# Optimization experiments

Hardware: AMD Instinct MI355X
Metric: run time of the kernel (lower is better)

The kernel has to match this reference:

```python
import jax, jax.numpy as jnp
import numpy as np


def setup_inputs() -> dict:
    key = jax.random.key(0)
    k1, k2, k3, k4 = jax.random.split(key, 4)
    T, IN, OUT = 4096, 4096, 4096  # tokens, in_features, out_features
    x = jax.random.normal(k1, (T, IN), dtype=jnp.float32)
    # simulated FP8 weight values (already quantized integers-ish codes stored as float)
    weight = jax.random.normal(k2, (OUT, IN), dtype=jnp.float32)
    # per-output-channel dequant scale
    weight_scale = jax.random.uniform(k3, (OUT,), dtype=jnp.float32, minval=0.01, maxval=0.1)
    bias = jax.random.normal(k4, (OUT,), dtype=jnp.float32)
    return {"x": x, "weight": weight, "weight_scale": weight_scale, "bias": bias}


def reference(x, weight, weight_scale, bias) -> jnp.ndarray:
    # FP8 quantized linear: dequantize weight with per-channel scale, then GEMM + bias.
    # weight: [out, in], weight_scale: [out], x: [tokens, in] -> out: [tokens, out]
    w_deq = weight * weight_scale[:, None]
    return jnp.einsum("ti,oi->to", x, w_deq) + bias
```

## Files before the change

kernel.cpp:

```cpp
#include <hip/hip_runtime.h>
#include <hip/hip_bf16.h>
#include <stdint.h>

typedef __bf16 bf16_t;
typedef bf16_t bf16x8 __attribute__((ext_vector_type(8)));
typedef float f32x4 __attribute__((ext_vector_type(4)));

#define BM 256
#define BN 256
#define BK 64

__device__ __forceinline__ void gload_lds16(const void* g, void* l) {
  __builtin_amdgcn_global_load_lds(
      (const __attribute__((address_space(1))) uint32_t*)g,
      (__attribute__((address_space(3))) uint32_t*)l, 16, 0, 0);
}

__global__ __launch_bounds__(256) void cvt_kernel(
    const float* __restrict__ x, bf16_t* __restrict__ xo, int n8x,
    const float* __restrict__ w, const float* __restrict__ scale,
    bf16_t* __restrict__ wo, int k8, int n8w, int gx) {
  if ((int)blockIdx.x < gx) {
    int stride = gx * blockDim.x;
    for (int i = blockIdx.x * blockDim.x + threadIdx.x; i < n8x; i += stride) {
      const f32x4* p = (const f32x4*)x + 2 * (size_t)i;
      f32x4 a = p[0], b = p[1];
      bf16x8 o;
#pragma unroll
      for (int r = 0; r < 4; ++r) { o[r] = (bf16_t)a[r]; o[r + 4] = (bf16_t)b[r]; }
      *((bf16x8*)xo + i) = o;
    }
  } else {
    int stride = (gridDim.x - gx) * blockDim.x;
    for (int i = (blockIdx.x - gx) * blockDim.x + threadIdx.x; i < n8w;
         i += stride) {
      int row = i / k8;
      float s = scale[row];
      const f32x4* p = (const f32x4*)w + 2 * (size_t)i;
      f32x4 a = p[0], b = p[1];
      bf16x8 o;
#pragma unroll
      for (int r = 0; r < 4; ++r) {
        o[r] = (bf16_t)(a[r] * s);
        o[r + 4] = (bf16_t)(b[r] * s);
      }
      *((bf16x8*)wo + i) = o;
    }
  }
}

__global__ __launch_bounds__(512, 2) void gemm256(
    const bf16_t* __restrict__ A, const bf16_t* __restrict__ B,
    const float* __restrict__ bias, float* __restrict__ C,
    int M, int N, int K) {
  __shared__ __attribute__((aligned(16))) char lds[131072];

  const int tid = threadIdx.x;
  const int lane = tid & 63;
  const int wave = tid >> 6;
  const int wm = wave >> 2;
  const int wn = wave & 3;

  int nwg = gridDim.x;
  int wg = blockIdx.x;
  if ((nwg & 7) == 0) { int cpx = nwg >> 3; wg = (wg & 7) * cpx + (wg >> 3); }
  const int ntn = N / BN;
  const int tm = wg / ntn;
  const int tn = wg % ntn;

  const size_t Kb = (size_t)K * 2;
  const char* gApan = (const char*)A + (size_t)tm * BM * Kb;
  const char* gBpan = (const char*)B + (size_t)tn * BN * Kb;

  const int xc = (((lane >> 4) ^ ((lane >> 1) & 3)) << 4);
  const int aBase = (wm * 128 + (lane & 15)) * 64 + xc;
  const int bBase = (wn * 64 + (lane & 15)) * 64 + xc;

  size_t srcoff[2];
  int ldst[2];
#pragma unroll
  for (int s = 0; s < 2; ++s) {
    int r = (wave * 2 + s) * 16 + (lane >> 2);
    int c = (lane & 3) ^ ((lane >> 3) & 3);
    srcoff[s] = (size_t)r * Kb + (size_t)(c << 4);
    ldst[s] = (wave * 2 + s) * 1024;
  }

#define STAGE_U(dstbase, pan, kbyte)                                          \
  {                                                                           \
    gload_lds16((pan) + srcoff[0] + (size_t)(kbyte), lds + (dstbase) + ldst[0]); \
    gload_lds16((pan) + srcoff[1] + (size_t)(kbyte), lds + (dstbase) + ldst[1]); \
  }
#define RD_A(dst, unitbase, ch)                                               \
  _Pragma("unroll") for (int i_ = 0; i_ < 4; ++i_)                            \
      dst[i_] = *(const bf16x8*)(lds + (unitbase) + aBase + (ch) * 4096 +     \
                                 i_ * 1024);
#define RD_B(dst, unitbase)                                                   \
  _Pragma("unroll") for (int j_ = 0; j_ < 4; ++j_)                            \
      dst[j_] = *(const bf16x8*)(lds + (unitbase) + bBase + j_ * 1024);
#define MFMA16(ab, bb_, accbase)                                              \
  __builtin_amdgcn_s_setprio(1);                                              \
  _Pragma("unroll") for (int i_ = 0; i_ < 4; ++i_)                            \
      _Pragma("unroll") for (int j_ = 0; j_ < 4; ++j_)                        \
          acc[(accbase) + i_][j_] = __builtin_amdgcn_mfma_f32_16x16x32_bf16(  \
              ab[i_], bb_[j_], acc[(accbase) + i_][j_], 0, 0, 0);             \
  __builtin_amdgcn_s_setprio(0);
#define WAIT_LGKM0() asm volatile("s_waitcnt lgkmcnt(0)" ::: "memory")
#define WAIT_VM(n)   asm volatile("s_waitcnt vmcnt(" #n ")" ::: "memory")
#define BAR()        __builtin_amdgcn_s_barrier()

  f32x4 acc[8][4];
#pragma unroll
  for (int a = 0; a < 8; ++a)
#pragma unroll
    for (int j = 0; j < 4; ++j) acc[a][j] = (f32x4)0.0f;

  const int NT = K / BK;

  STAGE_U(0,             gApan, 0);
  STAGE_U(32768,         gBpan, 0);
  STAGE_U(16384,         gApan, 64);
  STAGE_U(49152,         gBpan, 64);
  if (NT > 1) {
    STAGE_U(65536,         gApan, 128);
    STAGE_U(65536 + 32768, gBpan, 128);
    WAIT_VM(4);
  } else {
    WAIT_VM(0);
  }
  BAR();

  bf16x8 af[4], bf[4];

  for (int t = 0; t < NT; ++t) {
    const int bb = (t & 1) << 16;
    const int nb = bb ^ 65536;
    const size_t kb1 = (size_t)(t + 1) * 128;
    const size_t kb2 = (size_t)(t + 2) * 128;
    const bool st1 = (t + 1) < NT;
    const bool st2 = (t + 2) < NT;

    RD_A(af, bb, 0);
    RD_B(bf, bb + 32768);
    if (st1) STAGE_U(nb + 16384, gApan, kb1 + 64);
    BAR();
    WAIT_LGKM0();
    MFMA16(af, bf, 0);
    BAR();

    RD_A(af, bb, 1);
    if (st1) STAGE_U(nb + 49152, gBpan, kb1 + 64);
    BAR();
    WAIT_LGKM0();
    MFMA16(af, bf, 4);
    BAR();

    RD_A(af, bb + 16384, 0);
    RD_B(bf, bb + 49152);
    if (st2) STAGE_U(bb, gApan, kb2);
    BAR();
    WAIT_LGKM0();
    MFMA16(af, bf, 0);
    BAR();

    RD_A(af, bb + 16384, 1);
    if (st2) STAGE_U(bb + 32768, gBpan, kb2);
    BAR();
    WAIT_LGKM0();
    MFMA16(af, bf, 4);
    if (st2) { WAIT_VM(4); } else { WAIT_VM(0); }
    BAR();
  }
#undef STAGE_U
#undef RD_A
#undef RD_B
#undef MFMA16
#undef WAIT_LGKM0
#undef WAIT_VM
#undef BAR

  const int row0 = tm * BM + wm * 128;
  const int col0 = tn * BN + wn * 64;
#pragma unroll
  for (int j = 0; j < 4; ++j) {
    int c = col0 + j * 16 + (lane & 15);
    float bv = bias[c];
#pragma unroll
    for (int a = 0; a < 8; ++a) {
      int ch = a >> 2, i = a & 3;
      int rbase = row0 + ch * 64 + i * 16 + ((lane >> 4) << 2);
#pragma unroll
      for (int r = 0; r < 4; ++r)
        C[(size_t)(rbase + r) * N + c] = acc[a][j][r] + bv;
    }
  }
}

__global__ void fallback_gemm(const float* __restrict__ x,
                              const float* __restrict__ w,
                              const float* __restrict__ s,
                              const float* __restrict__ b,
                              float* __restrict__ out, int M, int N, int K) {
  int o = blockIdx.x * blockDim.x + threadIdx.x;
  if (o >= M * N) return;
  int m = o / N, n = o % N;
  const float* xr = x + (size_t)m * K;
  const float* wr = w + (size_t)n * K;
  float acc = 0.f;
  for (int k = 0; k < K; ++k) acc += xr[k] * wr[k];
  out[o] = acc * s[n] + b[n];
}

extern "C" void kernel_launch(void* const* d_in, const int* in_sizes, int n_in,
                              void* d_out, int out_size, void* d_ws,
                              size_t ws_size, hipStream_t stream) {
  const float* x = (const float*)d_in[0];
  const float* w = (const float*)d_in[1];
  const float* sc = (const float*)d_in[2];
  const float* bias = (const float*)d_in[3];
  float* out = (float*)d_out;

  const int N = in_sizes[2];
  const int K = in_sizes[1] / N;
  const int M = in_sizes[0] / K;

  const size_t need = ((size_t)M * K + (size_t)N * K) * sizeof(bf16_t);
  const bool fast = (ws_size >= need) && (M % BM == 0) && (N % BN == 0) &&
                    (K % BK == 0) && (K / BK >= 1);

  if (fast) {
    bf16_t* xb = (bf16_t*)d_ws;
    bf16_t* wb = xb + (size_t)M * K;

    int n8x = (M * K) / 8;
    int n8w = (N * K) / 8;
    const int gx = 2048;
    cvt_kernel<<<gx + 2048, 256, 0, stream>>>(x, xb, n8x, w, sc, wb, K / 8,
                                              n8w, gx);

    dim3 grid((M / BM) * (N / BN));
    gemm256<<<grid, 512, 0, stream>>>(xb, wb, bias, out, M, N, K);
  } else {
    int total = M * N;
    fallback_gemm<<<(total + 255) / 256, 256, 0, stream>>>(x, w, sc, bias, out,
                                                           M, N, K);
  }
}
```

Before: 158.9 us.

## Switch GEMM to 32x32x16 MFMA with double-buffered A fragments and fewer barriers

Replaces the 16x16x32 bf16 MFMA tiling with 32x32x16 instructions, which makes each wave issue fewer, larger MFMAs and read fewer LDS fragments per FLOP. The main loop is restructured from four barrier-separated phases into two. A-fragment register double buffering (aX/aY) prefetches the next k-slice's A operand while the current MFMAs run. Partial lgkmcnt waits and sched_barriers are used to keep LDS reads in flight. This adds register pressure from the extra A buffers and depends on the new swizzled LDS addressing being correct.

```diff
diff --git a/kernel.cpp b/kernel.cpp
--- a/kernel.cpp
+++ b/kernel.cpp
@@ -5,6 +5,7 @@
 typedef __bf16 bf16_t;
 typedef bf16_t bf16x8 __attribute__((ext_vector_type(8)));
 typedef float f32x4 __attribute__((ext_vector_type(4)));
+typedef float f32x16 __attribute__((ext_vector_type(16)));
 
 #define BM 256
 #define BN 256
@@ -72,9 +73,12 @@
   const char* gApan = (const char*)A + (size_t)tm * BM * Kb;
   const char* gBpan = (const char*)B + (size_t)tn * BN * Kb;
 
-  const int xc = (((lane >> 4) ^ ((lane >> 1) & 3)) << 4);
-  const int aBase = (wm * 128 + (lane & 15)) * 64 + xc;
-  const int bBase = (wn * 64 + (lane & 15)) * 64 + xc;
+  const int xs = (lane >> 1) & 3;
+  const int hi = lane >> 5;
+  const int cs0 = ((hi ^ xs) << 4);
+  const int cs1 = (((hi + 2) ^ xs) << 4);
+  const int aAddr = wm * 8192 + (lane & 31) * 64;
+  const int bAddr = wn * 4096 + (lane & 31) * 64;
 
   size_t srcoff[2];
   int ldst[2];
@@ -91,107 +95,111 @@
     gload_lds16((pan) + srcoff[0] + (size_t)(kbyte), lds + (dstbase) + ldst[0]); \
     gload_lds16((pan) + srcoff[1] + (size_t)(kbyte), lds + (dstbase) + ldst[1]); \
   }
-#define RD_A(dst, unitbase, ch)                                               \
-  _Pragma("unroll") for (int i_ = 0; i_ < 4; ++i_)                            \
-      dst[i_] = *(const bf16x8*)(lds + (unitbase) + aBase + (ch) * 4096 +     \
-                                 i_ * 1024);
-#define RD_B(dst, unitbase)                                                   \
-  _Pragma("unroll") for (int j_ = 0; j_ < 4; ++j_)                            \
-      dst[j_] = *(const bf16x8*)(lds + (unitbase) + bBase + j_ * 1024);
-#define MFMA16(ab, bb_, accbase)                                              \
+#define STAGE_K0(buf, tt)                                                     \
+  { STAGE_U((buf) + 0,     gApan, (size_t)(tt)*128);                          \
+    STAGE_U((buf) + 32768, gBpan, (size_t)(tt)*128); }
+#define STAGE_K1(buf, tt)                                                     \
+  { STAGE_U((buf) + 16384, gApan, (size_t)(tt)*128 + 64);                     \
+    STAGE_U((buf) + 49152, gBpan, (size_t)(tt)*128 + 64); }
+#define RD_B4(ub)                                                             \
+  _Pragma("unroll") for (int fc_ = 0; fc_ < 2; ++fc_) {                       \
+    bfr[fc_][0] = *(const bf16x8*)(lds + (ub) + bAddr + fc_ * 2048 + cs0);    \
+    bfr[fc_][1] = *(const bf16x8*)(lds + (ub) + bAddr + fc_ * 2048 + cs1);    \
+  }
+#define RD_A8(dst, ub)                                                        \
+  _Pragma("unroll") for (int fr_ = 0; fr_ < 4; ++fr_) {                       \
+    dst[fr_][0] = *(const bf16x8*)(lds + (ub) + aAddr + fr_ * 2048 + cs0);    \
+    dst[fr_][1] = *(const bf16x8*)(lds + (ub) + aAddr + fr_ * 2048 + cs1);    \
+  }
+#define MFMA16(aU)                                                            \
   __builtin_amdgcn_s_setprio(1);                                              \
-  _Pragma("unroll") for (int i_ = 0; i_ < 4; ++i_)                            \
-      _Pragma("unroll") for (int j_ = 0; j_ < 4; ++j_)                        \
-          acc[(accbase) + i_][j_] = __builtin_amdgcn_mfma_f32_16x16x32_bf16(  \
-              ab[i_], bb_[j_], acc[(accbase) + i_][j_], 0, 0, 0);             \
+  _Pragma("unroll") for (int fr_ = 0; fr_ < 4; ++fr_)                         \
+      _Pragma("unroll") for (int fc_ = 0; fc_ < 2; ++fc_) {                   \
+        acc[fr_][fc_] = __builtin_amdgcn_mfma_f32_32x32x16_bf16(              \
+            aU[fr_][0], bfr[fc_][0], acc[fr_][fc_], 0, 0, 0);                 \
+        acc[fr_][fc_] = __builtin_amdgcn_mfma_f32_32x32x16_bf16(              \
+            aU[fr_][1], bfr[fc_][1], acc[fr_][fc_], 0, 0, 0);                 \
+      }                                                                       \
   __builtin_amdgcn_s_setprio(0);
-#define WAIT_LGKM0() asm volatile("s_waitcnt lgkmcnt(0)" ::: "memory")
+#define WAIT_LGKM(n) asm volatile("s_waitcnt lgkmcnt(" #n ")" ::: "memory")
 #define WAIT_VM(n)   asm volatile("s_waitcnt vmcnt(" #n ")" ::: "memory")
+#define SCHED0()     __builtin_amdgcn_sched_barrier(0)
 #define BAR()        __builtin_amdgcn_s_barrier()
 
-  f32x4 acc[8][4];
-#pragma unroll
-  for (int a = 0; a < 8; ++a)
-#pragma unroll
-    for (int j = 0; j < 4; ++j) acc[a][j] = (f32x4)0.0f;
+  f32x16 acc[4][2];
+#pragma unroll
+  for (int fr = 0; fr < 4; ++fr)
+#pragma unroll
+    for (int fc = 0; fc < 2; ++fc) acc[fr][fc] = (f32x16)0.0f;
 
   const int NT = K / BK;
 
-  STAGE_U(0,             gApan, 0);
-  STAGE_U(32768,         gBpan, 0);
-  STAGE_U(16384,         gApan, 64);
-  STAGE_U(49152,         gBpan, 64);
+  STAGE_K0(0, 0);
+  STAGE_K1(0, 0);
   if (NT > 1) {
-    STAGE_U(65536,         gApan, 128);
-    STAGE_U(65536 + 32768, gBpan, 128);
+    STAGE_K0(65536, 1);
     WAIT_VM(4);
   } else {
     WAIT_VM(0);
   }
+  SCHED0();
   BAR();
 
-  bf16x8 af[4], bf[4];
+  bf16x8 aX[4][2], aY[4][2], bfr[2][2];
+  RD_A8(aX, 0);
 
   for (int t = 0; t < NT; ++t) {
     const int bb = (t & 1) << 16;
     const int nb = bb ^ 65536;
-    const size_t kb1 = (size_t)(t + 1) * 128;
-    const size_t kb2 = (size_t)(t + 2) * 128;
     const bool st1 = (t + 1) < NT;
     const bool st2 = (t + 2) < NT;
 
-    RD_A(af, bb, 0);
-    RD_B(bf, bb + 32768);
-    if (st1) STAGE_U(nb + 16384, gApan, kb1 + 64);
+    RD_B4(bb + 32768);
+    RD_A8(aY, bb + 16384);
+    if (st1) STAGE_K1(nb, t + 1);
+    WAIT_LGKM(8);
+    SCHED0();
+    MFMA16(aX);
+    if (st1) { WAIT_VM(4); } else { WAIT_VM(0); }
+    SCHED0();
     BAR();
-    WAIT_LGKM0();
-    MFMA16(af, bf, 0);
+
+    RD_B4(bb + 49152);
+    if (st1) RD_A8(aX, nb);
+    if (st2) STAGE_K0(bb, t + 2);
+    if (st1) { WAIT_LGKM(8); } else { WAIT_LGKM(0); }
+    SCHED0();
+    MFMA16(aY);
+    if (st2) { WAIT_VM(4); } else { WAIT_VM(0); }
+    SCHED0();
     BAR();
-
-    RD_A(af, bb, 1);
-    if (st1) STAGE_U(nb + 49152, gBpan, kb1 + 64);
-    BAR();
-    WAIT_LGKM0();
-    MFMA16(af, bf, 4);
-    BAR();
-
-    RD_A(af, bb + 16384, 0);
-    RD_B(bf, bb + 49152);
-    if (st2) STAGE_U(bb, gApan, kb2);
-    BAR();
-    WAIT_LGKM0();
-    MFMA16(af, bf, 0);
-    BAR();
-
-    RD_A(af, bb + 16384, 1);
-    if (st2) STAGE_U(bb + 32768, gBpan, kb2);
-    BAR();
-    WAIT_LGKM0();
-    MFMA16(af, bf, 4);
-    if (st2) { WAIT_VM(4); } else { WAIT_VM(0); }
-    BAR();
   }
 #undef STAGE_U
-#undef RD_A
-#undef RD_B
+#undef STAGE_K0
+#undef STAGE_K1
+#undef RD_B4
+#undef RD_A8
 #undef MFMA16
-#undef WAIT_LGKM0
+#undef WAIT_LGKM
 #undef WAIT_VM
+#undef SCHED0
 #undef BAR
 
   const int row0 = tm * BM + wm * 128;
   const int col0 = tn * BN + wn * 64;
-#pragma unroll
-  for (int j = 0; j < 4; ++j) {
-    int c = col0 + j * 16 + (lane & 15);
+  const int lrow = (lane >> 5) << 2;
+  const int lcol = lane & 31;
+#pragma unroll
+  for (int fc = 0; fc < 2; ++fc) {
+    int c = col0 + fc * 32 + lcol;
     float bv = bias[c];
 #pragma unroll
-    for (int a = 0; a < 8; ++a) {
-      int ch = a >> 2, i = a & 3;
-      int rbase = row0 + ch * 64 + i * 16 + ((lane >> 4) << 2);
-#pragma unroll
-      for (int r = 0; r < 4; ++r)
-        C[(size_t)(rbase + r) * N + c] = acc[a][j][r] + bv;
+    for (int fr = 0; fr < 4; ++fr) {
+#pragma unroll
+      for (int reg = 0; reg < 16; ++reg) {
+        int r = row0 + fr * 32 + (reg & 3) + ((reg >> 2) << 3) + lrow;
+        C[(size_t)r * N + c] = acc[fr][fc][reg] + bv;
+      }
     }
   }
 }
```

After: 172.6 us. 1.09x slower.

## Double-buffer LDS fragment registers to overlap reads with MFMA in GEMM loop

Applied to the files above, without the earlier changes.

Restructures the GEMM main loop to use two sets of A/B register fragments, so the LDS reads for the next MFMA block are issued before the current MFMA block runs. Full lgkmcnt(0) waits and one barrier per phase are replaced by partial waits and a single barrier. The loop is unrolled by two with precomputed LDS base pointers for each buffer, which requires an even tile count. The goal is to hide LDS read latency behind matrix math and cut synchronisation, at the cost of more registers and tighter ordering constraints.

```diff
diff --git a/kernel.cpp b/kernel.cpp
--- a/kernel.cpp
+++ b/kernel.cpp
@@ -75,6 +75,10 @@
   const int xc = (((lane >> 4) ^ ((lane >> 1) & 3)) << 4);
   const int aBase = (wm * 128 + (lane & 15)) * 64 + xc;
   const int bBase = (wn * 64 + (lane & 15)) * 64 + xc;
+  const char* pA0 = lds + aBase;
+  const char* pA1 = lds + 65536 + aBase;
+  const char* pB0 = lds + bBase;
+  const char* pB1 = lds + 65536 + bBase;
 
   size_t srcoff[2];
   int ldst[2];
@@ -86,18 +90,17 @@
     ldst[s] = (wave * 2 + s) * 1024;
   }
 
-#define STAGE_U(dstbase, pan, kbyte)                                          \
+#define STAGE_U(dstc, pan, kbyte)                                             \
   {                                                                           \
-    gload_lds16((pan) + srcoff[0] + (size_t)(kbyte), lds + (dstbase) + ldst[0]); \
-    gload_lds16((pan) + srcoff[1] + (size_t)(kbyte), lds + (dstbase) + ldst[1]); \
-  }
-#define RD_A(dst, unitbase, ch)                                               \
+    gload_lds16((pan) + srcoff[0] + (size_t)(kbyte), lds + (dstc) + ldst[0]); \
+    gload_lds16((pan) + srcoff[1] + (size_t)(kbyte), lds + (dstc) + ldst[1]); \
+  }
+#define RD_A(dst, P, u, ch)                                                   \
   _Pragma("unroll") for (int i_ = 0; i_ < 4; ++i_)                            \
-      dst[i_] = *(const bf16x8*)(lds + (unitbase) + aBase + (ch) * 4096 +     \
-                                 i_ * 1024);
-#define RD_B(dst, unitbase)                                                   \
+      dst[i_] = *(const bf16x8*)((P) + (u) + (ch) * 4096 + i_ * 1024);
+#define RD_B(dst, P, u)                                                       \
   _Pragma("unroll") for (int j_ = 0; j_ < 4; ++j_)                            \
-      dst[j_] = *(const bf16x8*)(lds + (unitbase) + bBase + j_ * 1024);
+      dst[j_] = *(const bf16x8*)((P) + (u) + j_ * 1024);
 #define MFMA16(ab, bb_, accbase)                                              \
   __builtin_amdgcn_s_setprio(1);                                              \
   _Pragma("unroll") for (int i_ = 0; i_ < 4; ++i_)                            \
@@ -105,9 +108,44 @@
           acc[(accbase) + i_][j_] = __builtin_amdgcn_mfma_f32_16x16x32_bf16(  \
               ab[i_], bb_[j_], acc[(accbase) + i_][j_], 0, 0, 0);             \
   __builtin_amdgcn_s_setprio(0);
-#define WAIT_LGKM0() asm volatile("s_waitcnt lgkmcnt(0)" ::: "memory")
+#define WAIT_LGKM(n) asm volatile("s_waitcnt lgkmcnt(" #n ")" ::: "memory")
 #define WAIT_VM(n)   asm volatile("s_waitcnt vmcnt(" #n ")" ::: "memory")
 #define BAR()        __builtin_amdgcn_s_barrier()
+
+#define TILE(t_, aBB, bBB, aNB, bNB, BBc, NBc)                                \
+  {                                                                           \
+    const bool st1 = (t_) + 1 < NT;                                           \
+    const bool st2 = (t_) + 2 < NT;                                           \
+    const size_t kb1 = (size_t)((t_) + 1) * 128;                              \
+    const size_t kb2 = (size_t)((t_) + 2) * 128;                              \
+                               \
+    if (st1) STAGE_U((NBc) + 16384, gApan, kb1 + 64);                         \
+    RD_A(aY, aBB, 0, 1);                                                      \
+    WAIT_LGKM(4);                                                             \
+    MFMA16(aX, b0, 0);                                                        \
+    BAR();                                                                    \
+                    \
+    if (st1) STAGE_U((NBc) + 49152, gBpan, kb1 + 64);                         \
+    RD_A(aX, aBB, 16384, 0);                                                  \
+    RD_B(b1, bBB, 49152);                                                     \
+    WAIT_LGKM(8);                                                             \
+    MFMA16(aY, b0, 4);                                                        \
+    BAR();                                                                    \
+                               \
+    if (st2) STAGE_U((BBc), gApan, kb2);                                      \
+    RD_A(aY, aBB, 16384, 1);                                                  \
+    WAIT_LGKM(4);                                                             \
+    MFMA16(aX, b1, 0);                                                        \
+    if (st2) { WAIT_VM(6); } else if (st1) { WAIT_VM(4); } else { WAIT_VM(0); } \
+    BAR();                                                                    \
+                           \
+    if (st2) STAGE_U((BBc) + 32768, gBpan, kb2);                              \
+    if (st1) { RD_A(aX, aNB, 0, 0); RD_B(b0, bNB, 32768); }                   \
+    if (st1) { WAIT_LGKM(8); } else { WAIT_LGKM(0); }                         \
+    MFMA16(aY, b1, 4);                                                        \
+    if (st2) { WAIT_VM(4); } else { WAIT_VM(0); }                             \
+    BAR();                                                                    \
+  }
 
   f32x4 acc[8][4];
 #pragma unroll
@@ -130,54 +168,22 @@
   }
   BAR();
 
-  bf16x8 af[4], bf[4];
-
-  for (int t = 0; t < NT; ++t) {
-    const int bb = (t & 1) << 16;
-    const int nb = bb ^ 65536;
-    const size_t kb1 = (size_t)(t + 1) * 128;
-    const size_t kb2 = (size_t)(t + 2) * 128;
-    const bool st1 = (t + 1) < NT;
-    const bool st2 = (t + 2) < NT;
-
-    RD_A(af, bb, 0);
-    RD_B(bf, bb + 32768);
-    if (st1) STAGE_U(nb + 16384, gApan, kb1 + 64);
-    BAR();
-    WAIT_LGKM0();
-    MFMA16(af, bf, 0);
-    BAR();
-
-    RD_A(af, bb, 1);
-    if (st1) STAGE_U(nb + 49152, gBpan, kb1 + 64);
-    BAR();
-    WAIT_LGKM0();
-    MFMA16(af, bf, 4);
-    BAR();
-
-    RD_A(af, bb + 16384, 0);
-    RD_B(bf, bb + 49152);
-    if (st2) STAGE_U(bb, gApan, kb2);
-    BAR();
-    WAIT_LGKM0();
-    MFMA16(af, bf, 0);
-    BAR();
-
-    RD_A(af, bb + 16384, 1);
-    if (st2) STAGE_U(bb + 32768, gBpan, kb2);
-    BAR();
-    WAIT_LGKM0();
-    MFMA16(af, bf, 4);
-    if (st2) { WAIT_VM(4); } else { WAIT_VM(0); }
-    BAR();
+  bf16x8 aX[4], aY[4], b0[4], b1[4];
+  RD_A(aX, pA0, 0, 0);
+  RD_B(b0, pB0, 32768);
+
+  for (int t = 0; t < NT; t += 2) {
+    TILE(t,     pA0, pB0, pA1, pB1, 0,     65536);
+    TILE(t + 1, pA1, pB1, pA0, pB0, 65536, 0);
   }
 #undef STAGE_U
 #undef RD_A
 #undef RD_B
 #undef MFMA16
-#undef WAIT_LGKM0
+#undef WAIT_LGKM
 #undef WAIT_VM
 #undef BAR
+#undef TILE
 
   const int row0 = tm * BM + wm * 128;
   const int col0 = tn * BN + wn * 64;
@@ -225,8 +231,9 @@
   const int M = in_sizes[0] / K;
 
   const size_t need = ((size_t)M * K + (size_t)N * K) * sizeof(bf16_t);
+  const int NT = K / BK;
   const bool fast = (ws_size >= need) && (M % BM == 0) && (N % BN == 0) &&
-                    (K % BK == 0) && (K / BK >= 1);
+                    (K % BK == 0) && (NT >= 2) && (NT % 2 == 0);
 
   if (fast) {
     bf16_t* xb = (bf16_t*)d_ws;
```

Measured after the change: 225.1 us. 41.7% more time.

## Restructure GEMM LDS layout to 128-byte rows and reorder quadrant MFMA schedule

Applied to the files above, without the earlier changes.

Changes the LDS tile layout from 64-byte K-half units to full 128-byte rows covering BK=64, split by row halves, with an 8-way XOR swizzle. Each fragment read now loads both K halves, and the main loop computes in four quadrants that reuse A and B fragments, so the final quadrant runs without a preceding LDS read and overlaps the next-stage prefetch. The goal is fewer LDS reads and barriers per iteration and better overlap of global-to-LDS loads. The cost is more live fragment registers, and the changed staging order could introduce hazards.

```diff
diff --git a/kernel.cpp b/kernel.cpp
--- a/kernel.cpp
+++ b/kernel.cpp
@@ -71,41 +71,61 @@
   const size_t Kb = (size_t)K * 2;
   const char* gApan = (const char*)A + (size_t)tm * BM * Kb;
   const char* gBpan = (const char*)B + (size_t)tn * BN * Kb;
-
-  const int xc = (((lane >> 4) ^ ((lane >> 1) & 3)) << 4);
-  const int aBase = (wm * 128 + (lane & 15)) * 64 + xc;
-  const int bBase = (wn * 64 + (lane & 15)) * 64 + xc;
+  const size_t rowHi = (size_t)128 * Kb;
+
+  const int l7 = lane & 7;
+  const int hi = lane >> 4;
+  const int c0b = ((hi ^ l7) << 4);
+  const int c1b = (((hi + 4) ^ l7) << 4);
+  const int aB0 = wm * 16384 + (lane & 15) * 128 + c0b;
+  const int aB1 = wm * 16384 + (lane & 15) * 128 + c1b;
+  const int bB0 = 32768 + (wn >> 1) * 16384 + (wn & 1) * 8192 +
+                  (lane & 15) * 128 + c0b;
+  const int bB1 = 32768 + (wn >> 1) * 16384 + (wn & 1) * 8192 +
+                  (lane & 15) * 128 + c1b;
 
   size_t srcoff[2];
   int ldst[2];
 #pragma unroll
   for (int s = 0; s < 2; ++s) {
-    int r = (wave * 2 + s) * 16 + (lane >> 2);
-    int c = (lane & 3) ^ ((lane >> 3) & 3);
-    srcoff[s] = (size_t)r * Kb + (size_t)(c << 4);
+    int row_l = (wave * 2 + s) * 8 + (lane >> 3);
+    int csrc = (lane & 7) ^ ((lane >> 3) & 7);
+    srcoff[s] = (size_t)row_l * Kb + (size_t)(csrc << 4);
     ldst[s] = (wave * 2 + s) * 1024;
   }
 
-#define STAGE_U(dstbase, pan, kbyte)                                          \
+#define STAGE_U(dstc, pan, rowoff, kbyte)                                     \
   {                                                                           \
-    gload_lds16((pan) + srcoff[0] + (size_t)(kbyte), lds + (dstbase) + ldst[0]); \
-    gload_lds16((pan) + srcoff[1] + (size_t)(kbyte), lds + (dstbase) + ldst[1]); \
-  }
-#define RD_A(dst, unitbase, ch)                                               \
-  _Pragma("unroll") for (int i_ = 0; i_ < 4; ++i_)                            \
-      dst[i_] = *(const bf16x8*)(lds + (unitbase) + aBase + (ch) * 4096 +     \
-                                 i_ * 1024);
-#define RD_B(dst, unitbase)                                                   \
-  _Pragma("unroll") for (int j_ = 0; j_ < 4; ++j_)                            \
-      dst[j_] = *(const bf16x8*)(lds + (unitbase) + bBase + j_ * 1024);
-#define MFMA16(ab, bb_, accbase)                                              \
+    gload_lds16((pan) + (rowoff) + srcoff[0] + (size_t)(kbyte),               \
+                lds + (dstc) + ldst[0]);                                      \
+    gload_lds16((pan) + (rowoff) + srcoff[1] + (size_t)(kbyte),               \
+                lds + (dstc) + ldst[1]);                                      \
+  }
+#define RD_A(r_)                                                              \
+  _Pragma("unroll") for (int i_ = 0; i_ < 4; ++i_) {                          \
+    af[i_][0] = *(const bf16x8*)(Lb + aB0 + (r_) * 8192 + i_ * 2048);         \
+    af[i_][1] = *(const bf16x8*)(Lb + aB1 + (r_) * 8192 + i_ * 2048);         \
+  }
+#define RD_BC(dst, c_)                                                        \
+  _Pragma("unroll") for (int j_ = 0; j_ < 2; ++j_) {                          \
+    dst[j_][0] = *(const bf16x8*)(Lb + bB0 + (c_) * 4096 + j_ * 2048);        \
+    dst[j_][1] = *(const bf16x8*)(Lb + bB1 + (c_) * 4096 + j_ * 2048);        \
+  }
+#define MFMAQ(r_, c_, bset)                                                   \
   __builtin_amdgcn_s_setprio(1);                                              \
   _Pragma("unroll") for (int i_ = 0; i_ < 4; ++i_)                            \
-      _Pragma("unroll") for (int j_ = 0; j_ < 4; ++j_)                        \
-          acc[(accbase) + i_][j_] = __builtin_amdgcn_mfma_f32_16x16x32_bf16(  \
-              ab[i_], bb_[j_], acc[(accbase) + i_][j_], 0, 0, 0);             \
+      _Pragma("unroll") for (int j_ = 0; j_ < 2; ++j_) {                      \
+        acc[(r_) * 4 + i_][(c_) * 2 + j_] =                                   \
+            __builtin_amdgcn_mfma_f32_16x16x32_bf16(                          \
+                af[i_][0], bset[j_][0], acc[(r_) * 4 + i_][(c_) * 2 + j_],    \
+                0, 0, 0);                                                     \
+        acc[(r_) * 4 + i_][(c_) * 2 + j_] =                                   \
+            __builtin_amdgcn_mfma_f32_16x16x32_bf16(                          \
+                af[i_][1], bset[j_][1], acc[(r_) * 4 + i_][(c_) * 2 + j_],    \
+                0, 0, 0);                                                     \
+      }                                                                       \
   __builtin_amdgcn_s_setprio(0);
-#define WAIT_LGKM0() asm volatile("s_waitcnt lgkmcnt(0)" ::: "memory")
+#define WAIT_LGKM(n) asm volatile("s_waitcnt lgkmcnt(" #n ")" ::: "memory")
 #define WAIT_VM(n)   asm volatile("s_waitcnt vmcnt(" #n ")" ::: "memory")
 #define BAR()        __builtin_amdgcn_s_barrier()
 
@@ -117,65 +137,65 @@
 
   const int NT = K / BK;
 
-  STAGE_U(0,             gApan, 0);
-  STAGE_U(32768,         gBpan, 0);
-  STAGE_U(16384,         gApan, 64);
-  STAGE_U(49152,         gBpan, 64);
+  STAGE_U(0,     gApan, 0,     0);
+  STAGE_U(16384, gApan, rowHi, 0);
+  STAGE_U(32768, gBpan, 0,     0);
+  STAGE_U(49152, gBpan, rowHi, 0);
   if (NT > 1) {
-    STAGE_U(65536,         gApan, 128);
-    STAGE_U(65536 + 32768, gBpan, 128);
+    STAGE_U(65536,         gApan, 0, 128);
+    STAGE_U(65536 + 32768, gBpan, 0, 128);
     WAIT_VM(4);
   } else {
     WAIT_VM(0);
   }
   BAR();
 
-  bf16x8 af[4], bf[4];
+  bf16x8 af[4][2], b0[2][2], b1[2][2];
 
   for (int t = 0; t < NT; ++t) {
     const int bb = (t & 1) << 16;
     const int nb = bb ^ 65536;
+    const char* Lb = lds + bb;
     const size_t kb1 = (size_t)(t + 1) * 128;
     const size_t kb2 = (size_t)(t + 2) * 128;
     const bool st1 = (t + 1) < NT;
     const bool st2 = (t + 2) < NT;
 
-    RD_A(af, bb, 0);
-    RD_B(bf, bb + 32768);
-    if (st1) STAGE_U(nb + 16384, gApan, kb1 + 64);
-    BAR();
-    WAIT_LGKM0();
-    MFMA16(af, bf, 0);
-    BAR();
-
-    RD_A(af, bb, 1);
-    if (st1) STAGE_U(nb + 49152, gBpan, kb1 + 64);
-    BAR();
-    WAIT_LGKM0();
-    MFMA16(af, bf, 4);
-    BAR();
-
-    RD_A(af, bb + 16384, 0);
-    RD_B(bf, bb + 49152);
-    if (st2) STAGE_U(bb, gApan, kb2);
-    BAR();
-    WAIT_LGKM0();
-    MFMA16(af, bf, 0);
-    BAR();
-
-    RD_A(af, bb + 16384, 1);
-    if (st2) STAGE_U(bb + 32768, gBpan, kb2);
-    BAR();
-    WAIT_LGKM0();
-    MFMA16(af, bf, 4);
+    RD_A(0);
+    RD_BC(b0, 0);
+    if (st1) STAGE_U(nb + 16384, gApan, rowHi, kb1);
+    WAIT_LGKM(8);
+    BAR();
+    WAIT_LGKM(0);
+    MFMAQ(0, 0, b0);
+    BAR();
+
+    RD_BC(b1, 1);
+    if (st1) STAGE_U(nb + 49152, gBpan, rowHi, kb1);
+    BAR();
+    WAIT_LGKM(0);
+    MFMAQ(0, 1, b1);
+    BAR();
+
+    RD_A(1);
+    BAR();
+    WAIT_LGKM(0);
+    MFMAQ(1, 1, b1);
+    BAR();
+
+    if (st2) {
+      STAGE_U(bb,         gApan, 0, kb2);
+      STAGE_U(bb + 32768, gBpan, 0, kb2);
+    }
+    MFMAQ(1, 0, b0);
     if (st2) { WAIT_VM(4); } else { WAIT_VM(0); }
     BAR();
   }
 #undef STAGE_U
 #undef RD_A
-#undef RD_B
-#undef MFMA16
-#undef WAIT_LGKM0
+#undef RD_BC
+#undef MFMAQ
+#undef WAIT_LGKM
 #undef WAIT_VM
 #undef BAR
 
```

New measurement: 152.8 us. 3.8% less time.
